# Optimization experiments

Hardware: AMD Instinct MI355X
Metric: run time of the kernel (lower is better)

Reference implementation:

```python
import jax, jax.numpy as jnp
import numpy as np

# OpenCV GaussianBlur with ksize=3, sigma=0 uses the fixed small-kernel table
# [0.25, 0.5, 0.25] (separable), with border mode BORDER_REFLECT_101, which
# corresponds to jnp.pad(mode='reflect').
K0, K1 = 0.25, 0.5

def setup_inputs() -> dict:
    key = jax.random.key(0)
    x = jax.random.normal(key, (64, 3, 512, 512), dtype=jnp.float32)
    return {"x": x}

def _blur(x):
    # x: [B, C, H, W]; separable 1-2-1 / 4 filter along H then W.
    xp = jnp.pad(x, ((0, 0), (0, 0), (1, 1), (0, 0)), mode='reflect')
    x = K0 * xp[:, :, :-2, :] + K1 * xp[:, :, 1:-1, :] + K0 * xp[:, :, 2:, :]
    xp = jnp.pad(x, ((0, 0), (0, 0), (0, 0), (1, 1)), mode='reflect')
    x = K0 * xp[:, :, :, :-2] + K1 * xp[:, :, :, 1:-1] + K0 * xp[:, :, :, 2:]
    return x

def reference(x):
    return _blur(x)
```

## Files before the change

kernel.cpp:

```cpp
#include <hip/hip_runtime.h>


#define HH 512
#define WW 512

typedef float f4 __attribute__((ext_vector_type(4)));

#define VBLUR(d, m, c, pq)                         \
    d.x = 0.25f * (m.x + pq.x) + 0.5f * c.x;       \
    d.y = 0.25f * (m.y + pq.y) + 0.5f * c.y;       \
    d.z = 0.25f * (m.z + pq.z) + 0.5f * c.z;       \
    d.w = 0.25f * (m.w + pq.w) + 0.5f * c.w;

#define HBLUR(oa, ob, ua, ub, l, r)                \
    oa.x = 0.25f * (l    + ua.y) + 0.5f * ua.x;    \
    oa.y = 0.25f * (ua.x + ua.z) + 0.5f * ua.y;    \
    oa.z = 0.25f * (ua.y + ua.w) + 0.5f * ua.z;    \
    oa.w = 0.25f * (ua.z + ub.x) + 0.5f * ua.w;    \
    ob.x = 0.25f * (ua.w + ub.y) + 0.5f * ub.x;    \
    ob.y = 0.25f * (ub.x + ub.z) + 0.5f * ub.y;    \
    ob.z = 0.25f * (ub.y + ub.w) + 0.5f * ub.z;    \
    ob.w = 0.25f * (ub.z + r   ) + 0.5f * ub.w;

#define ROW_FINISH(ua, ub, h)                                        \
    {                                                                \
        float l = __shfl_up(ub.w, 1);                                \
        float r = __shfl_down(ua.x, 1);                              \
        if (lane == 0)  l = ua.y;                                    \
        if (lane == 63) r = ub.z;                                    \
        f4 oa, ob;                                                   \
        HBLUR(oa, ob, ua, ub, l, r)                                  \
        f4* S = (f4*)(q + (size_t)(h) * WW + w0);                    \
        __builtin_nontemporal_store(oa, S);                          \
        __builtin_nontemporal_store(ob, S + 1);                      \
    }

__global__ __launch_bounds__(256) void gauss3_kernel(const float* __restrict__ in,
                                                     float* __restrict__ out) {
    int wid  = (blockIdx.x * 256 + threadIdx.x) >> 6;
    int lane = threadIdx.x & 63;

    int quad  = wid & 127;
    int plane = wid >> 7;

    int h0 = quad << 2;
    int hm = (h0 == 0)       ? 1      : h0 - 1;
    int hp = (h0 + 4 == HH)  ? HH - 2 : h0 + 4;

    const float* p = in  + (size_t)plane * (HH * WW);
    float*       q = out + (size_t)plane * (HH * WW);
    int w0 = lane << 3;

    const f4* Lm = (const f4*)(p + (size_t)hm       * WW + w0);
    const f4* L0 = (const f4*)(p + (size_t)h0       * WW + w0);
    const f4* L1 = (const f4*)(p + (size_t)(h0 + 1) * WW + w0);
    const f4* L2 = (const f4*)(p + (size_t)(h0 + 2) * WW + w0);
    const f4* L3 = (const f4*)(p + (size_t)(h0 + 3) * WW + w0);
    const f4* Lp = (const f4*)(p + (size_t)hp       * WW + w0);

    f4 ama = Lm[0], amb = Lm[1];
    f4 a0a = L0[0], a0b = L0[1];
    f4 a1a = L1[0], a1b = L1[1];
    f4 a2a = L2[0], a2b = L2[1];
    f4 a3a = L3[0], a3b = L3[1];
    f4 apa = Lp[0], apb = Lp[1];

    f4 ua, ub;
    VBLUR(ua, ama, a0a, a1a)  VBLUR(ub, amb, a0b, a1b)
    ROW_FINISH(ua, ub, h0)
    VBLUR(ua, a0a, a1a, a2a)  VBLUR(ub, a0b, a1b, a2b)
    ROW_FINISH(ua, ub, h0 + 1)
    VBLUR(ua, a1a, a2a, a3a)  VBLUR(ub, a1b, a2b, a3b)
    ROW_FINISH(ua, ub, h0 + 2)
    VBLUR(ua, a2a, a3a, apa)  VBLUR(ub, a2b, a3b, apb)
    ROW_FINISH(ua, ub, h0 + 3)
}

extern "C" void kernel_launch(void* const* d_in, const int* in_sizes, int n_in,
                              void* d_out, int out_size, void* d_ws, size_t ws_size,
                              hipStream_t stream) {
    const float* x   = (const float*)d_in[0];
    float*       out = (float*)d_out;

    int n      = in_sizes[0];
    int planes = n / (HH * WW);
    int waves  = planes * (HH / 4);
    int blocks = waves / 4;

    gauss3_kernel<<<blocks, 256, 0, stream>>>(x, out);
}
```

Measured before the change: 76.40 us.

## Stage 16-row strips with halo into LDS via direct global-to-LDS loads

Each 256-thread block now owns a 16-row strip of one plane. It copies the strip plus its two halo rows into shared memory with asynchronous global-to-LDS loads, then each wave blurs four rows from LDS. This cuts redundant halo-row global reads from six rows per four outputs to eighteen per sixteen. The cost is a 36 KB LDS footprint per block, which lowers occupancy, plus a block-wide barrier that serialises load and compute within each block.

```diff
diff --git a/kernel.cpp b/kernel.cpp
--- a/kernel.cpp
+++ b/kernel.cpp
@@ -3,6 +3,8 @@
 
 #define HH 512
 #define WW 512
+#define STRIP 16
+#define SROWS (STRIP + 2)
 
 typedef float f4 __attribute__((ext_vector_type(4)));
 
@@ -22,7 +24,7 @@
     ob.z = 0.25f * (ub.y + ub.w) + 0.5f * ub.z;    \
     ob.w = 0.25f * (ub.z + r   ) + 0.5f * ub.w;
 
-#define ROW_FINISH(ua, ub, h)                                        \
+#define ROW_FINISH(ua, ub, S)                                        \
     {                                                                \
         float l = __shfl_up(ub.w, 1);                                \
         float r = __shfl_down(ua.x, 1);                              \
@@ -30,33 +32,53 @@
         if (lane == 63) r = ub.z;                                    \
         f4 oa, ob;                                                   \
         HBLUR(oa, ob, ua, ub, l, r)                                  \
-        f4* S = (f4*)(q + (size_t)(h) * WW + w0);                    \
-        __builtin_nontemporal_store(oa, S);                          \
-        __builtin_nontemporal_store(ob, S + 1);                      \
+        __builtin_nontemporal_store(oa, (S));                        \
+        __builtin_nontemporal_store(ob, (S) + 1);                    \
     }
 
 __global__ __launch_bounds__(256) void gauss3_kernel(const float* __restrict__ in,
                                                      float* __restrict__ out) {
-    int wid  = (blockIdx.x * 256 + threadIdx.x) >> 6;
-    int lane = threadIdx.x & 63;
+    __shared__ float lds[SROWS * WW];
 
-    int quad  = wid & 127;
-    int plane = wid >> 7;
+    int bid   = blockIdx.x;
+    int plane = bid >> 5;
+    int strip = bid & 31;
+    int h0    = strip << 4;
+    int row_start = (h0 == 0) ? 0 : h0 - 1;
 
-    int h0 = quad << 2;
-    int hm = (h0 == 0)       ? 1      : h0 - 1;
-    int hp = (h0 + 4 == HH)  ? HH - 2 : h0 + 4;
+    int tid  = threadIdx.x;
+    int lane = tid & 63;
+    int wv   = tid >> 6;
 
     const float* p = in  + (size_t)plane * (HH * WW);
     float*       q = out + (size_t)plane * (HH * WW);
+
+#pragma unroll
+    for (int i = 0; i < (SROWS * WW) / 1024; ++i) {
+        int o    = i * 1024 + tid * 4;
+        int rrel = o >> 9;
+        int col  = o & (WW - 1);
+        int grow = row_start + rrel;
+        if (grow > HH - 1) grow = HH - 1;
+        const float* src = p + (size_t)grow * WW + col;
+        __builtin_amdgcn_global_load_lds(
+            (const __attribute__((address_space(1))) void*)src,
+            (__attribute__((address_space(3))) void*)(lds + o),
+            16, 0, 0);
+    }
+    __syncthreads();
+
+    int g0 = h0 + (wv << 2);
+    int gm = (g0 == 0)       ? 1      : g0 - 1;
+    int gp = (g0 + 4 == HH)  ? HH - 2 : g0 + 4;
+
     int w0 = lane << 3;
-
-    const f4* Lm = (const f4*)(p + (size_t)hm       * WW + w0);
-    const f4* L0 = (const f4*)(p + (size_t)h0       * WW + w0);
-    const f4* L1 = (const f4*)(p + (size_t)(h0 + 1) * WW + w0);
-    const f4* L2 = (const f4*)(p + (size_t)(h0 + 2) * WW + w0);
-    const f4* L3 = (const f4*)(p + (size_t)(h0 + 3) * WW + w0);
-    const f4* Lp = (const f4*)(p + (size_t)hp       * WW + w0);
+    const f4* Lm = (const f4*)(lds + (gm         - row_start) * WW + w0);
+    const f4* L0 = (const f4*)(lds + (g0         - row_start) * WW + w0);
+    const f4* L1 = (const f4*)(lds + (g0 + 1     - row_start) * WW + w0);
+    const f4* L2 = (const f4*)(lds + (g0 + 2     - row_start) * WW + w0);
+    const f4* L3 = (const f4*)(lds + (g0 + 3     - row_start) * WW + w0);
+    const f4* Lp = (const f4*)(lds + (gp         - row_start) * WW + w0);
 
     f4 ama = Lm[0], amb = Lm[1];
     f4 a0a = L0[0], a0b = L0[1];
@@ -65,15 +87,16 @@
     f4 a3a = L3[0], a3b = L3[1];
     f4 apa = Lp[0], apb = Lp[1];
 
+    float* qb = q + w0;
     f4 ua, ub;
     VBLUR(ua, ama, a0a, a1a)  VBLUR(ub, amb, a0b, a1b)
-    ROW_FINISH(ua, ub, h0)
+    ROW_FINISH(ua, ub, (f4*)(qb + (size_t)g0       * WW))
     VBLUR(ua, a0a, a1a, a2a)  VBLUR(ub, a0b, a1b, a2b)
-    ROW_FINISH(ua, ub, h0 + 1)
+    ROW_FINISH(ua, ub, (f4*)(qb + (size_t)(g0 + 1) * WW))
     VBLUR(ua, a1a, a2a, a3a)  VBLUR(ub, a1b, a2b, a3b)
-    ROW_FINISH(ua, ub, h0 + 2)
+    ROW_FINISH(ua, ub, (f4*)(qb + (size_t)(g0 + 2) * WW))
     VBLUR(ua, a2a, a3a, apa)  VBLUR(ub, a2b, a3b, apb)
-    ROW_FINISH(ua, ub, h0 + 3)
+    ROW_FINISH(ua, ub, (f4*)(qb + (size_t)(g0 + 3) * WW))
 }
 
 extern "C" void kernel_launch(void* const* d_in, const int* in_sizes, int n_in,
@@ -84,8 +107,6 @@
 
     int n      = in_sizes[0];
     int planes = n / (HH * WW);
-    int waves  = planes * (HH / 4);
-    int blocks = waves / 4;
-
+    int blocks = planes * (HH / STRIP);
     gauss3_kernel<<<blocks, 256, 0, stream>>>(x, out);
 }
```

Result: slower. 91.24 us (+19.4%).
